# Performance work log

Measured on AMD Instinct MI355X. Metric: run time of the kernel, lower is better.

Reference implementation:

```python
import jax, jax.numpy as jnp
import numpy as np

B, D, ND, K = 4096, 16384, 32, 8  # batch, input_size, num_domains, k
NUM_CLASSES = 2


def setup_inputs() -> dict:
    key = jax.random.key(0)
    k1, k2, k3, k4, k5, k6 = jax.random.split(key, 6)
    x = jax.random.normal(k1, (B, D), dtype=jnp.float32)
    domains = jax.random.randint(k2, (B,), 0, ND)
    # parameters, initialized as in the torch module
    sms = 0.1 * jax.random.normal(k3, (K + 1, D, NUM_CLASSES), dtype=jnp.float32)
    sm_biases = 0.1 * jax.random.normal(k4, (K + 1, NUM_CLASSES), dtype=jnp.float32)
    embs = 1e-4 * jax.random.normal(k5, (ND, K), dtype=jnp.float32)
    cs_wt = 0.1 + 1e-4 * jax.random.normal(k6, (), dtype=jnp.float32)
    return {"x": x, "domains": domains, "sms": sms, "sm_biases": sm_biases,
            "embs": embs, "cs_wt": cs_wt}


def reference(x, domains, sms, sm_biases, embs, cs_wt):
    # x: [B, D], sms: [K+1, D, C], sm_biases: [K+1, C], embs: [ND, K]
    Bsz = x.shape[0]
    # Project x through all K+1 small classifiers once: [B, K+1, C].
    # (Algebraic reordering of einsum('bk,krl->brl') then ('brl,br->bl'):
    #  avoids the [B, D, C] intermediate; identical math.)
    proj = jnp.einsum('bd,kdc->bkc', x, sms)
    logits_common = proj[:, 0, :] + sm_biases[0]
    # per-sample component weights
    c_wts = jnp.concatenate(
        [jnp.full((Bsz, 1), 1.0, dtype=x.dtype) * cs_wt, embs[domains]], axis=1)
    c_wts = jnp.tanh(c_wts)  # [B, K+1]
    logits_specialized = jnp.einsum('bk,bkc->bc', c_wts, proj) + c_wts @ sm_biases
    # orthogonality regularizer on the component weight matrices
    cps = jnp.einsum('kdc,jdc->ckj', sms, sms)  # [C, K+1, K+1]
    eye = jnp.eye(K + 1, dtype=sms.dtype)[None]
    orth_loss = jnp.mean((cps - eye) ** 2)
    return logits_specialized, logits_common, orth_loss
```

## Files before the change

### kernel.cpp

```cpp
#include <hip/hip_runtime.h>
#include <hip/hip_bf16.h>
#include <cmath>

#define B_SZ 4096
#define D_SZ 16384
#define NKC 18
#define W2_STRIDE 32
#define RB 64
#define TD 128

__global__ void rearrange_w(const float* __restrict__ sms, float* __restrict__ w2) {
    int idx = blockIdx.x * 256 + threadIdx.x;
    if (idx >= D_SZ * NKC) return;
    int d = idx / NKC, j = idx % NKC;
    int k = j >> 1, c = j & 1;
    w2[(size_t)d * W2_STRIDE + j] = sms[(size_t)k * D_SZ * 2 + (size_t)d * 2 + c];
}

__global__ __launch_bounds__(256, 4) void proj_main(
    const float* __restrict__ x, const float* __restrict__ w2,
    float* __restrict__ part, int nrowgrp, int dseg) {
    __shared__ float tile[RB * TD];

    int rb  = (blockIdx.x % nrowgrp) * RB;
    int seg = blockIdx.x / nrowgrp;
    int d0  = seg * dseg;
    int tid  = threadIdx.x;
    int lane = tid & 63;
    int wave = __builtin_amdgcn_readfirstlane(tid >> 6);

    float acc[NKC];
#pragma unroll
    for (int j = 0; j < NKC; j++) acc[j] = 0.f;

    const int rswz = (lane & 7) << 2;

    for (int t = 0; t < dseg; t += TD) {
        __syncthreads();
#pragma unroll
        for (int i = 0; i < 8; i++) {
            int flat = i * 1024 + tid * 4;
            int row  = flat >> 7;
            int dd   = flat & 127;
            float4 v = *reinterpret_cast<const float4*>(
                &x[(size_t)(rb + row) * D_SZ + d0 + t + dd]);
            int wswz = (row & 7) << 2;
            *reinterpret_cast<float4*>(&tile[row * TD + (dd ^ wswz)]) = v;
        }
        __syncthreads();
        int base = wave * 32;
        for (int u = 0; u < 8; u++) {
            int dd = base + u * 4;
            float4 xv = *reinterpret_cast<const float4*>(
                &tile[lane * TD + (dd ^ rswz)]);
            const float* w = &w2[(size_t)(d0 + t + dd) * W2_STRIDE];
            float xq[4] = {xv.x, xv.y, xv.z, xv.w};
#pragma unroll
            for (int q = 0; q < 4; q++) {
#pragma unroll
                for (int j = 0; j < NKC; j++)
                    acc[j] = fmaf(xq[q], w[q * W2_STRIDE + j], acc[j]);
            }
        }
    }

    __syncthreads();
#pragma unroll
    for (int j = 0; j < NKC; j++)
        tile[(wave * 64 + lane) * NKC + j] = acc[j];
    __syncthreads();
    if (wave == 0) {
#pragma unroll
        for (int j = 0; j < NKC; j++) {
            float s = tile[lane * NKC + j] + tile[(64 + lane) * NKC + j]
                    + tile[(128 + lane) * NKC + j] + tile[(192 + lane) * NKC + j];
            part[((size_t)seg * B_SZ + rb + lane) * NKC + j] = s;
        }
    }
}

__global__ void orth_kernel(const float* __restrict__ sms, float* __restrict__ orth) {
    int b = blockIdx.x;
    int c = b / 81;
    int k = (b / 9) % 9;
    int j = b % 9;
    const float* pk = sms + (size_t)k * D_SZ * 2 + c;
    const float* pj = sms + (size_t)j * D_SZ * 2 + c;
    float s = 0.f;
    for (int d = threadIdx.x; d < D_SZ; d += 256)
        s += pk[(size_t)d * 2] * pj[(size_t)d * 2];
    for (int off = 32; off; off >>= 1) s += __shfl_down(s, off, 64);
    __shared__ float sd[4];
    int lane = threadIdx.x & 63, wave = threadIdx.x >> 6;
    if (lane == 0) sd[wave] = s;
    __syncthreads();
    if (threadIdx.x == 0) {
        float dot = sd[0] + sd[1] + sd[2] + sd[3];
        float v = dot - (k == j ? 1.0f : 0.0f);
        orth[b] = v * v;
    }
}

__global__ void epilogue(const float* __restrict__ part,
                         const float* __restrict__ sm_biases,
                         const float* __restrict__ embs,
                         const int* __restrict__ domains,
                         const float* __restrict__ cs_wt,
                         const float* __restrict__ orth,
                         float* __restrict__ out, int segs) {
    int row = blockIdx.x * 256 + threadIdx.x;
    if (row < B_SZ) {
        float proj[NKC];
#pragma unroll
        for (int j = 0; j < NKC; j++) proj[j] = 0.f;
        for (int s = 0; s < segs; s++) {
#pragma unroll
            for (int j = 0; j < NKC; j++)
                proj[j] += part[((size_t)s * B_SZ + row) * NKC + j];
        }
        int dom = domains[row];
        float cw[9];
        cw[0] = tanhf(cs_wt[0]);
#pragma unroll
        for (int k = 1; k < 9; k++) cw[k] = tanhf(embs[dom * 8 + (k - 1)]);
        float s0 = 0.f, s1 = 0.f;
#pragma unroll
        for (int k = 0; k < 9; k++) {
            s0 += cw[k] * (proj[2 * k]     + sm_biases[2 * k]);
            s1 += cw[k] * (proj[2 * k + 1] + sm_biases[2 * k + 1]);
        }
        out[(size_t)row * 2 + 0] = s0;
        out[(size_t)row * 2 + 1] = s1;
        out[2 * B_SZ + (size_t)row * 2 + 0] = proj[0] + sm_biases[0];
        out[2 * B_SZ + (size_t)row * 2 + 1] = proj[1] + sm_biases[1];
    }
    if (blockIdx.x == 0 && threadIdx.x == 0) {
        float l = 0.f;
        for (int e = 0; e < 162; e++) l += orth[e];
        out[4 * B_SZ] = l / 162.f;
    }
}

extern "C" void kernel_launch(void* const* d_in, const int* in_sizes, int n_in,
                              void* d_out, int out_size, void* d_ws, size_t ws_size,
                              hipStream_t stream) {
    const float* x         = (const float*)d_in[0];
    const int*   domains   = (const int*)d_in[1];
    const float* sms       = (const float*)d_in[2];
    const float* sm_biases = (const float*)d_in[3];
    const float* embs      = (const float*)d_in[4];
    const float* cs_wt     = (const float*)d_in[5];
    float* out = (float*)d_out;

    float* w2 = (float*)d_ws;
    size_t w2_elems = (size_t)D_SZ * W2_STRIDE;
    int segs = 16;
    while (segs > 1 &&
           (w2_elems + (size_t)segs * B_SZ * NKC + 162) * 4 > ws_size)
        segs >>= 1;
    float* part = w2 + w2_elems;
    float* orth = part + (size_t)segs * B_SZ * NKC;
    int dseg = D_SZ / segs;
    int nrowgrp = B_SZ / RB;

    rearrange_w<<<(D_SZ * NKC + 255) / 256, 256, 0, stream>>>(sms, w2);
    proj_main<<<nrowgrp * segs, 256, 0, stream>>>(x, w2, part, nrowgrp, dseg);
    orth_kernel<<<162, 256, 0, stream>>>(sms, orth);
    epilogue<<<(B_SZ + 255) / 256, 256, 0, stream>>>(
        part, sm_biases, embs, domains, cs_wt, orth, out, segs);
}
```

Before: 451.0 us.

## Keep weights in registers and stream x rows with shuffle-transpose reductions

The projection kernel is restructured so that each thread holds a 4-wide slice of all 18 weight columns in registers and streams x rows past them. Per-row partial dots are reduced across the wavefront with a butterfly shuffle-transpose that scatters the 18 outputs over lanes. This removes the weight rearrangement kernel and the LDS tiling of x. The orthogonality computation is rewritten to use only the symmetric upper triangle, split across D with atomics, and merged into the epilogue. The cost is heavy register use (72 weight registers) and a long shuffle chain for every row.

```diff
diff --git a/kernel.cpp b/kernel.cpp
--- a/kernel.cpp
+++ b/kernel.cpp
@@ -5,140 +5,196 @@
 #define B_SZ 4096
 #define D_SZ 16384
 #define NKC 18
-#define W2_STRIDE 32
-#define RB 64
-#define TD 128
-
-__global__ void rearrange_w(const float* __restrict__ sms, float* __restrict__ w2) {
-    int idx = blockIdx.x * 256 + threadIdx.x;
-    if (idx >= D_SZ * NKC) return;
-    int d = idx / NKC, j = idx % NKC;
-    int k = j >> 1, c = j & 1;
-    w2[(size_t)d * W2_STRIDE + j] = sms[(size_t)k * D_SZ * 2 + (size_t)d * 2 + c];
-}
-
-__global__ __launch_bounds__(256, 4) void proj_main(
-    const float* __restrict__ x, const float* __restrict__ w2,
-    float* __restrict__ part, int nrowgrp, int dseg) {
-    __shared__ float tile[RB * TD];
-
-    int rb  = (blockIdx.x % nrowgrp) * RB;
-    int seg = blockIdx.x / nrowgrp;
-    int d0  = seg * dseg;
-    int tid  = threadIdx.x;
-    int lane = tid & 63;
-    int wave = __builtin_amdgcn_readfirstlane(tid >> 6);
-
-    float acc[NKC];
-#pragma unroll
-    for (int j = 0; j < NKC; j++) acc[j] = 0.f;
-
-    const int rswz = (lane & 7) << 2;
-
-    for (int t = 0; t < dseg; t += TD) {
-        __syncthreads();
-#pragma unroll
-        for (int i = 0; i < 8; i++) {
-            int flat = i * 1024 + tid * 4;
-            int row  = flat >> 7;
-            int dd   = flat & 127;
-            float4 v = *reinterpret_cast<const float4*>(
-                &x[(size_t)(rb + row) * D_SZ + d0 + t + dd]);
-            int wswz = (row & 7) << 2;
-            *reinterpret_cast<float4*>(&tile[row * TD + (dd ^ wswz)]) = v;
-        }
-        __syncthreads();
-        int base = wave * 32;
-        for (int u = 0; u < 8; u++) {
-            int dd = base + u * 4;
-            float4 xv = *reinterpret_cast<const float4*>(
-                &tile[lane * TD + (dd ^ rswz)]);
-            const float* w = &w2[(size_t)(d0 + t + dd) * W2_STRIDE];
-            float xq[4] = {xv.x, xv.y, xv.z, xv.w};
-#pragma unroll
-            for (int q = 0; q < 4; q++) {
-#pragma unroll
-                for (int j = 0; j < NKC; j++)
-                    acc[j] = fmaf(xq[q], w[q * W2_STRIDE + j], acc[j]);
-            }
-        }
-    }
-
+
+template <bool ATOMIC>
+__global__ void proj_stream(const float* __restrict__ x,
+                            const float* __restrict__ sms,
+                            float* __restrict__ part) {
+    const int bid  = blockIdx.x;
+    const int dblk = bid & 15;
+    const int r0   = (bid >> 4) * 64;
+    const int tid  = threadIdx.x;
+    const int lane = tid & 63;
+    const int wave = tid >> 6;
+    const int dbase = dblk * 1024 + wave * 256 + lane * 4;
+
+    float wr[72];
+#pragma unroll
+    for (int k = 0; k < 9; ++k)
+#pragma unroll
+        for (int q = 0; q < 4; ++q) {
+            const float2 wv = *reinterpret_cast<const float2*>(
+                sms + (size_t)k * (D_SZ * 2) + (size_t)(dbase + q) * 2);
+            wr[q * 18 + k * 2 + 0] = wv.x;
+            wr[q * 18 + k * 2 + 1] = wv.y;
+        }
+
+    int start = 0, len = 9;
+    if (lane & 2)  { start += 5; len -= 5; } else { len = len < 5 ? len : 5; }
+    if (lane & 4)  { start += 3; len -= 3; } else { len = len < 3 ? len : 3; }
+    if (lane & 8)  { start += 2; len -= 2; } else { len = len < 2 ? len : 2; }
+    if (lane & 16) { start += 1; len -= 1; } else { len = len < 1 ? len : 1; }
+    const bool valid = (len >= 1) && (lane < 32) && (start <= 8);
+    const int  kj    = start * 2 + (lane & 1);
+
+    __shared__ float stage[4][16][NKC];
+    const float* xrow = x + (size_t)r0 * D_SZ + dbase;
+
+    for (int bt = 0; bt < 4; ++bt) {
+#pragma unroll 2
+        for (int rl = 0; rl < 16; ++rl) {
+            const int rr = bt * 16 + rl;
+            const float4 xv =
+                *reinterpret_cast<const float4*>(xrow + (size_t)rr * D_SZ);
+            float acc[18];
+#pragma unroll
+            for (int j = 0; j < 18; ++j) acc[j] = xv.x * wr[j];
+#pragma unroll
+            for (int j = 0; j < 18; ++j) acc[j] = fmaf(xv.y, wr[18 + j], acc[j]);
+#pragma unroll
+            for (int j = 0; j < 18; ++j) acc[j] = fmaf(xv.z, wr[36 + j], acc[j]);
+#pragma unroll
+            for (int j = 0; j < 18; ++j) acc[j] = fmaf(xv.w, wr[54 + j], acc[j]);
+
+            float v[10];
+#pragma unroll
+            for (int i = 0; i < 9; ++i) {
+                float send = (lane & 1) ? acc[2 * i] : acc[2 * i + 1];
+                float r = __shfl_xor(send, 1, 64);
+                v[i] = ((lane & 1) ? acc[2 * i + 1] : acc[2 * i]) + r;
+            }
+            v[9] = 0.f;
+            float v2[6];
+#pragma unroll
+            for (int i = 0; i < 5; ++i) {
+                float send = (lane & 2) ? v[i] : v[5 + i];
+                float r = __shfl_xor(send, 2, 64);
+                v2[i] = ((lane & 2) ? v[5 + i] : v[i]) + r;
+            }
+            v2[5] = 0.f;
+            float v3[4];
+#pragma unroll
+            for (int i = 0; i < 3; ++i) {
+                float send = (lane & 4) ? v2[i] : v2[3 + i];
+                float r = __shfl_xor(send, 4, 64);
+                v3[i] = ((lane & 4) ? v2[3 + i] : v2[i]) + r;
+            }
+            v3[3] = 0.f;
+            float v4[2];
+#pragma unroll
+            for (int i = 0; i < 2; ++i) {
+                float send = (lane & 8) ? v3[i] : v3[2 + i];
+                float r = __shfl_xor(send, 8, 64);
+                v4[i] = ((lane & 8) ? v3[2 + i] : v3[i]) + r;
+            }
+            float send5 = (lane & 16) ? v4[0] : v4[1];
+            float r5 = __shfl_xor(send5, 16, 64);
+            float s = ((lane & 16) ? v4[1] : v4[0]) + r5;
+            s += __shfl_xor(s, 32, 64);
+
+            if (ATOMIC) {
+                if (valid)
+                    atomicAdd(&part[(size_t)(r0 + rr) * NKC + kj], s);
+            } else {
+                if (valid) stage[wave][rl][kj] = s;
+            }
+        }
+        if (!ATOMIC) {
+            __syncthreads();
+            for (int idx = tid; idx < 16 * NKC; idx += 256) {
+                const int rl = idx / NKC, jj = idx % NKC;
+                const float sum = stage[0][rl][jj] + stage[1][rl][jj] +
+                                  stage[2][rl][jj] + stage[3][rl][jj];
+                part[((size_t)dblk * B_SZ + (r0 + bt * 16 + rl)) * NKC + jj] = sum;
+            }
+            __syncthreads();
+        }
+    }
+}
+
+__global__ void orth_partial(const float* __restrict__ sms,
+                             float* __restrict__ dots) {
+    const int p = blockIdx.x >> 2;
+    const int dseg = blockIdx.x & 3;
+    int k = 0, rem = p;
+    while (rem >= 9 - k) { rem -= 9 - k; ++k; }
+    const int j = k + rem;
+    const int tid = threadIdx.x;
+    const float* rk = sms + (size_t)k * (D_SZ * 2);
+    const float* rj = sms + (size_t)j * (D_SZ * 2);
+    float d0 = 0.f, d1 = 0.f;
+    const int dbase = dseg * 4096;
+#pragma unroll 4
+    for (int i = 0; i < 16; ++i) {
+        const int d = dbase + i * 256 + tid;
+        const float2 a = *reinterpret_cast<const float2*>(rk + (size_t)d * 2);
+        const float2 b = *reinterpret_cast<const float2*>(rj + (size_t)d * 2);
+        d0 = fmaf(a.x, b.x, d0);
+        d1 = fmaf(a.y, b.y, d1);
+    }
+    for (int m = 32; m; m >>= 1) {
+        d0 += __shfl_xor(d0, m, 64);
+        d1 += __shfl_xor(d1, m, 64);
+    }
+    __shared__ float sd[8];
+    const int lane = tid & 63, wv = tid >> 6;
+    if (lane == 0) { sd[wv * 2] = d0; sd[wv * 2 + 1] = d1; }
     __syncthreads();
-#pragma unroll
-    for (int j = 0; j < NKC; j++)
-        tile[(wave * 64 + lane) * NKC + j] = acc[j];
-    __syncthreads();
-    if (wave == 0) {
-#pragma unroll
-        for (int j = 0; j < NKC; j++) {
-            float s = tile[lane * NKC + j] + tile[(64 + lane) * NKC + j]
-                    + tile[(128 + lane) * NKC + j] + tile[(192 + lane) * NKC + j];
-            part[((size_t)seg * B_SZ + rb + lane) * NKC + j] = s;
-        }
-    }
-}
-
-__global__ void orth_kernel(const float* __restrict__ sms, float* __restrict__ orth) {
-    int b = blockIdx.x;
-    int c = b / 81;
-    int k = (b / 9) % 9;
-    int j = b % 9;
-    const float* pk = sms + (size_t)k * D_SZ * 2 + c;
-    const float* pj = sms + (size_t)j * D_SZ * 2 + c;
-    float s = 0.f;
-    for (int d = threadIdx.x; d < D_SZ; d += 256)
-        s += pk[(size_t)d * 2] * pj[(size_t)d * 2];
-    for (int off = 32; off; off >>= 1) s += __shfl_down(s, off, 64);
-    __shared__ float sd[4];
-    int lane = threadIdx.x & 63, wave = threadIdx.x >> 6;
-    if (lane == 0) sd[wave] = s;
-    __syncthreads();
-    if (threadIdx.x == 0) {
-        float dot = sd[0] + sd[1] + sd[2] + sd[3];
-        float v = dot - (k == j ? 1.0f : 0.0f);
-        orth[b] = v * v;
-    }
-}
-
-__global__ void epilogue(const float* __restrict__ part,
-                         const float* __restrict__ sm_biases,
-                         const float* __restrict__ embs,
-                         const int* __restrict__ domains,
-                         const float* __restrict__ cs_wt,
-                         const float* __restrict__ orth,
-                         float* __restrict__ out, int segs) {
-    int row = blockIdx.x * 256 + threadIdx.x;
-    if (row < B_SZ) {
-        float proj[NKC];
-#pragma unroll
-        for (int j = 0; j < NKC; j++) proj[j] = 0.f;
-        for (int s = 0; s < segs; s++) {
-#pragma unroll
-            for (int j = 0; j < NKC; j++)
-                proj[j] += part[((size_t)s * B_SZ + row) * NKC + j];
-        }
-        int dom = domains[row];
-        float cw[9];
-        cw[0] = tanhf(cs_wt[0]);
-#pragma unroll
-        for (int k = 1; k < 9; k++) cw[k] = tanhf(embs[dom * 8 + (k - 1)]);
-        float s0 = 0.f, s1 = 0.f;
-#pragma unroll
-        for (int k = 0; k < 9; k++) {
-            s0 += cw[k] * (proj[2 * k]     + sm_biases[2 * k]);
-            s1 += cw[k] * (proj[2 * k + 1] + sm_biases[2 * k + 1]);
-        }
-        out[(size_t)row * 2 + 0] = s0;
-        out[(size_t)row * 2 + 1] = s1;
-        out[2 * B_SZ + (size_t)row * 2 + 0] = proj[0] + sm_biases[0];
-        out[2 * B_SZ + (size_t)row * 2 + 1] = proj[1] + sm_biases[1];
-    }
-    if (blockIdx.x == 0 && threadIdx.x == 0) {
-        float l = 0.f;
-        for (int e = 0; e < 162; e++) l += orth[e];
-        out[4 * B_SZ] = l / 162.f;
-    }
+    if (tid == 0) {
+        atomicAdd(&dots[p * 2 + 0], sd[0] + sd[2] + sd[4] + sd[6]);
+        atomicAdd(&dots[p * 2 + 1], sd[1] + sd[3] + sd[5] + sd[7]);
+    }
+}
+
+template <int SLICES>
+__global__ void epilogue2(const float* __restrict__ part,
+                          const float* __restrict__ sm_biases,
+                          const float* __restrict__ embs,
+                          const int* __restrict__ domains,
+                          const float* __restrict__ cs_wt,
+                          const float* __restrict__ dots,
+                          float* __restrict__ out) {
+    if (blockIdx.x == 16) {
+        const int lane = threadIdx.x;
+        if (lane >= 64) return;
+        float prt = 0.f;
+        if (lane < 45) {
+            int k = 0, rem = lane;
+            while (rem >= 9 - k) { rem -= 9 - k; ++k; }
+            const int j = k + rem;
+            const float e = (k == j) ? 1.f : 0.f;
+            const float m = (k == j) ? 1.f : 2.f;
+            const float a = dots[lane * 2] - e;
+            const float b = dots[lane * 2 + 1] - e;
+            prt = m * (a * a + b * b);
+        }
+        for (int mm = 32; mm; mm >>= 1) prt += __shfl_xor(prt, mm, 64);
+        if (lane == 0) out[4 * B_SZ] = prt / 162.f;
+        return;
+    }
+    const int row = blockIdx.x * 256 + threadIdx.x;
+    float proj[18];
+#pragma unroll
+    for (int jj = 0; jj < 18; ++jj) proj[jj] = 0.f;
+    for (int sl = 0; sl < SLICES; ++sl)
+#pragma unroll
+        for (int jj = 0; jj < 18; ++jj)
+            proj[jj] += part[((size_t)sl * B_SZ + row) * NKC + jj];
+    const int dom = domains[row];
+    float cw[9];
+    cw[0] = tanhf(cs_wt[0]);
+#pragma unroll
+    for (int k = 1; k < 9; ++k) cw[k] = tanhf(embs[dom * 8 + k - 1]);
+    float s0 = 0.f, s1 = 0.f;
+#pragma unroll
+    for (int k = 0; k < 9; ++k) {
+        s0 += cw[k] * (proj[2 * k]     + sm_biases[2 * k]);
+        s1 += cw[k] * (proj[2 * k + 1] + sm_biases[2 * k + 1]);
+    }
+    out[(size_t)row * 2 + 0] = s0;
+    out[(size_t)row * 2 + 1] = s1;
+    out[2 * B_SZ + (size_t)row * 2 + 0] = proj[0] + sm_biases[0];
+    out[2 * B_SZ + (size_t)row * 2 + 1] = proj[1] + sm_biases[1];
 }
 
 extern "C" void kernel_launch(void* const* d_in, const int* in_sizes, int n_in,
@@ -152,20 +208,24 @@
     const float* cs_wt     = (const float*)d_in[5];
     float* out = (float*)d_out;
 
-    float* w2 = (float*)d_ws;
-    size_t w2_elems = (size_t)D_SZ * W2_STRIDE;
-    int segs = 16;
-    while (segs > 1 &&
-           (w2_elems + (size_t)segs * B_SZ * NKC + 162) * 4 > ws_size)
-        segs >>= 1;
-    float* part = w2 + w2_elems;
-    float* orth = part + (size_t)segs * B_SZ * NKC;
-    int dseg = D_SZ / segs;
-    int nrowgrp = B_SZ / RB;
-
-    rearrange_w<<<(D_SZ * NKC + 255) / 256, 256, 0, stream>>>(sms, w2);
-    proj_main<<<nrowgrp * segs, 256, 0, stream>>>(x, w2, part, nrowgrp, dseg);
-    orth_kernel<<<162, 256, 0, stream>>>(sms, orth);
-    epilogue<<<(B_SZ + 255) / 256, 256, 0, stream>>>(
-        part, sm_biases, embs, domains, cs_wt, orth, out, segs);
-}
+    const size_t staged_elems = (size_t)16 * B_SZ * NKC;
+    const bool   staged = ws_size >= (staged_elems + 90) * sizeof(float);
+
+    if (staged) {
+        float* part = (float*)d_ws;
+        float* dots = part + staged_elems;
+        hipMemsetAsync(dots, 0, 90 * sizeof(float), stream);
+        proj_stream<false><<<1024, 256, 0, stream>>>(x, sms, part);
+        orth_partial<<<180, 256, 0, stream>>>(sms, dots);
+        epilogue2<16><<<17, 256, 0, stream>>>(part, sm_biases, embs, domains,
+                                              cs_wt, dots, out);
+    } else {
+        float* accb = (float*)d_ws;
+        float* dots = accb + (size_t)B_SZ * NKC;
+        hipMemsetAsync(accb, 0, ((size_t)B_SZ * NKC + 90) * sizeof(float), stream);
+        proj_stream<true><<<1024, 256, 0, stream>>>(x, sms, accb);
+        orth_partial<<<180, 256, 0, stream>>>(sms, dots);
+        epilogue2<1><<<17, 256, 0, stream>>>(accb, sm_biases, embs, domains,
+                                             cs_wt, dots, out);
+    }
+}
```

Measured after the change: 403.2 us. 10.6% less time.
